# Kernel optimization log

Measured on AMD Instinct MI355X. Metric: run time of the kernel, lower is better.

The kernel has to match this reference:

```python
import jax, jax.numpy as jnp
import numpy as np

N_NODES = 50000
N_EDGES = 1600000
IN_FEAT = 256
HID = IN_FEAT // 2  # 128
OUT_FEAT = 256


def setup_inputs() -> dict:
    key = jax.random.key(0)
    ks = jax.random.split(key, 10)
    x = jax.random.normal(ks[0], (N_NODES, IN_FEAT), dtype=jnp.float32)
    w = jax.random.uniform(ks[1], (N_EDGES, 1), dtype=jnp.float32)
    src = jax.random.randint(ks[2], (N_EDGES,), 0, N_NODES, dtype=jnp.int32)
    dst = jax.random.randint(ks[3], (N_EDGES,), 0, N_NODES, dtype=jnp.int32)
    s = 1.0 / np.sqrt(IN_FEAT)
    W_node = jax.random.uniform(ks[4], (IN_FEAT, HID), jnp.float32, -s, s)
    b_node = jax.random.uniform(ks[5], (HID,), jnp.float32, -s, s)
    W_edge = jax.random.uniform(ks[6], (IN_FEAT, HID), jnp.float32, -s, s)
    b_edge = jax.random.uniform(ks[7], (HID,), jnp.float32, -s, s)
    s2 = 1.0 / np.sqrt(HID)
    W_mlp = jax.random.uniform(ks[8], (HID, OUT_FEAT), jnp.float32, -s2, s2)
    b_mlp = jax.random.uniform(ks[9], (OUT_FEAT,), jnp.float32, -s2, s2)
    return {"x": x, "w": w, "src": src, "dst": dst,
            "W_node": W_node, "b_node": b_node,
            "W_edge": W_edge, "b_edge": b_edge,
            "W_mlp": W_mlp, "b_mlp": b_mlp}


def reference(x, w, src, dst, W_node, b_node, W_edge, b_edge, W_mlp, b_mlp):
    # message[v] = sum_{(u->v) in E} x[u] * w_e   (src_mul_edge + sum)
    message = jax.ops.segment_sum(x[src] * w, dst, num_segments=x.shape[0])  # [N, in_feat]
    h = (x @ W_node + b_node) + (message @ W_edge + b_edge)  # [N, in_feat//2]
    # NOTE: original uses nn.LeakyReLU(True) -> negative_slope=1.0 (identity);
    # replicated faithfully.
    h = jax.nn.leaky_relu(h, negative_slope=1.0)
    return h @ W_mlp + b_mlp  # [N, out_feat]
```

## Files before the change

kernel.cpp:

```cpp
#include <hip/hip_runtime.h>


constexpr int N_NODES  = 50000;
constexpr int N_EDGES  = 1600000;
constexpr int IN_FEAT  = 256;
constexpr int HID      = 128;
constexpr int OUT_FEAT = 256;

constexpr int BIN_SZ   = 32;
constexpr int N_BINS   = (N_NODES + BIN_SZ - 1) / BIN_SZ;
constexpr int CAPBIN   = 1536;
constexpr int EPB      = 4096;
constexpr int N_CBLK   = (N_EDGES + EPB - 1) / EPB;

typedef __attribute__((ext_vector_type(8))) short bf16x8;
typedef __attribute__((ext_vector_type(4))) float f32x4;

static __device__ __forceinline__ unsigned short f2bf(float f) {
    unsigned u = __builtin_bit_cast(unsigned, f);
    u += 0x7FFF + ((u >> 16) & 1);
    return (unsigned short)(u >> 16);
}
static __device__ __forceinline__ float bflo(unsigned u) {
    return __builtin_bit_cast(float, u << 16);
}
static __device__ __forceinline__ float bfhi(unsigned u) {
    return __builtin_bit_cast(float, u & 0xFFFF0000u);
}

__global__ __launch_bounds__(256) void k0_convert(
    const float* __restrict__ Wn, const float* __restrict__ We,
    const float* __restrict__ Wm,
    unsigned short* __restrict__ Wcat_t, unsigned short* __restrict__ Wmt)
{
    int n = blockIdx.x;
    int k = threadIdx.x;
    float v = (n < HID) ? Wn[(size_t)k * HID + n] : We[(size_t)k * HID + (n - HID)];
    Wcat_t[(size_t)n * IN_FEAT + k] = f2bf(v);
    if (k < HID) Wmt[(size_t)n * HID + k] = f2bf(Wm[(size_t)k * OUT_FEAT + n]);
}

__global__ __launch_bounds__(512) void binC(
    const int* __restrict__ src, const int* __restrict__ dst,
    const float* __restrict__ w, int* __restrict__ cursor,
    int2* __restrict__ entries)
{
    __shared__ int  hist[N_BINS];
    __shared__ int  gbase[N_BINS];
    __shared__ int  wsum[8];
    __shared__ int  stot;
    __shared__ int2 sorted[EPB];

    const int t = threadIdx.x;
    const int wave = t >> 6, lane = t & 63;
    const int e0 = blockIdx.x * EPB;

    for (int i = t; i < N_BINS; i += 512) hist[i] = 0;
    __syncthreads();

    int meta[8], wb[8], rk[8], bn[8];
    #pragma unroll
    for (int k = 0; k < 8; ++k) {
        int e = e0 + t + k * 512;
        bn[k] = -1;
        if (e < N_EDGES) {
            int d = dst[e];
            int b = d >> 5;
            bn[k]   = b;
            meta[k] = src[e] | ((d & 31) << 16) | (b << 21);
            wb[k]   = __float_as_int(w[e]);
            rk[k]   = atomicAdd(&hist[b], 1);
        }
    }
    __syncthreads();

    const int b4 = t * 4;
    int c0 = 0, c1 = 0, c2 = 0, c3 = 0;
    if (b4 + 0 < N_BINS) c0 = hist[b4 + 0];
    if (b4 + 1 < N_BINS) c1 = hist[b4 + 1];
    if (b4 + 2 < N_BINS) c2 = hist[b4 + 2];
    if (b4 + 3 < N_BINS) c3 = hist[b4 + 3];
    const int s = c0 + c1 + c2 + c3;
    int pre = s;
    #pragma unroll
    for (int off = 1; off < 64; off <<= 1) {
        int o = __shfl_up(pre, off, 64);
        if (lane >= off) pre += o;
    }
    if (lane == 63) wsum[wave] = pre;
    __syncthreads();
    if (t == 0) {
        int r = 0;
        #pragma unroll
        for (int q = 0; q < 8; ++q) { int v = wsum[q]; wsum[q] = r; r += v; }
        stot = r;
    }
    __syncthreads();
    const int tb = wsum[wave] + pre - s;

    if (b4 + 0 < N_BINS) {
        hist[b4 + 0]  = tb;
        gbase[b4 + 0] = c0 ? atomicAdd(&cursor[b4 + 0], c0) : 0;
    }
    if (b4 + 1 < N_BINS) {
        hist[b4 + 1]  = tb + c0;
        gbase[b4 + 1] = c1 ? atomicAdd(&cursor[b4 + 1], c1) : 0;
    }
    if (b4 + 2 < N_BINS) {
        hist[b4 + 2]  = tb + c0 + c1;
        gbase[b4 + 2] = c2 ? atomicAdd(&cursor[b4 + 2], c2) : 0;
    }
    if (b4 + 3 < N_BINS) {
        hist[b4 + 3]  = tb + c0 + c1 + c2;
        gbase[b4 + 3] = c3 ? atomicAdd(&cursor[b4 + 3], c3) : 0;
    }
    __syncthreads();

    #pragma unroll
    for (int k = 0; k < 8; ++k)
        if (bn[k] >= 0)
            sorted[hist[bn[k]] + rk[k]] = make_int2(meta[k], wb[k]);
    __syncthreads();

    const int tot = stot;
    #pragma unroll
    for (int k = 0; k < 8; ++k) {
        int i = t + k * 512;
        if (i < tot) {
            int2 q = sorted[i];
            int b = ((unsigned)q.x) >> 21;
            int r = i - hist[b];
            int g = gbase[b] + r;
            if (g < CAPBIN)
                entries[(size_t)b * CAPBIN + g] = make_int2(q.x & 0x1FFFFF, q.y);
        }
    }
}

__global__ __launch_bounds__(512) void gatherB(
    const unsigned short* __restrict__ ybf, const float* __restrict__ h0,
    const int* __restrict__ cursor, const int2* __restrict__ entries,
    unsigned short* __restrict__ hbf)
{
    __shared__ int2 sorted[CAPBIN];
    __shared__ int  cnt32[BIN_SZ];
    __shared__ int  offs32[BIN_SZ];

    const int t = threadIdx.x;
    const int bin = blockIdx.x;
    const int node0 = bin * BIN_SZ;
    const int wave = t >> 6, lane = t & 63;

    const int tot = min(cursor[bin], CAPBIN);
    if (t < BIN_SZ) cnt32[t] = 0;
    __syncthreads();

    int2 held[3];
    int  hrank[3], hdloc[3];
    #pragma unroll
    for (int k = 0; k < 3; ++k) {
        hdloc[k] = -1;
        int g = t + k * 512;
        if (g < tot) {
            int2 ep = entries[(size_t)bin * CAPBIN + g];
            int dloc = ep.x >> 16;
            held[k]  = make_int2(ep.x & 0xFFFF, ep.y);
            hdloc[k] = dloc;
            hrank[k] = atomicAdd(&cnt32[dloc], 1);
        }
    }
    __syncthreads();

    if (wave == 0) {
        int v = (lane < BIN_SZ) ? cnt32[lane] : 0;
        int sum = v;
        #pragma unroll
        for (int off = 1; off < BIN_SZ; off <<= 1) {
            int o = __shfl_up(sum, off, 64);
            if (lane >= off) sum += o;
        }
        if (lane < BIN_SZ) offs32[lane] = sum - v;
    }
    __syncthreads();

    #pragma unroll
    for (int k = 0; k < 3; ++k)
        if (hdloc[k] >= 0)
            sorted[offs32[hdloc[k]] + hrank[k]] = held[k];
    __syncthreads();

    #pragma unroll
    for (int n4 = 0; n4 < 4; ++n4) {
        const int nl = wave * 4 + n4;
        const int node = node0 + nl;
        const int beg = offs32[nl];
        const int c = cnt32[nl];
        float a0 = 0.f, a1 = 0.f;
        int j = 0;
        for (; j + 4 <= c; j += 4) {
            int2 q0 = sorted[beg + j];
            int2 q1 = sorted[beg + j + 1];
            int2 q2 = sorted[beg + j + 2];
            int2 q3 = sorted[beg + j + 3];
            unsigned u0 = *(const unsigned*)&ybf[(size_t)q0.x * HID + 2 * lane];
            unsigned u1 = *(const unsigned*)&ybf[(size_t)q1.x * HID + 2 * lane];
            unsigned u2 = *(const unsigned*)&ybf[(size_t)q2.x * HID + 2 * lane];
            unsigned u3 = *(const unsigned*)&ybf[(size_t)q3.x * HID + 2 * lane];
            float w0 = __int_as_float(q0.y), w1 = __int_as_float(q1.y);
            float w2 = __int_as_float(q2.y), w3 = __int_as_float(q3.y);
            a0 += w0 * bflo(u0); a1 += w0 * bfhi(u0);
            a0 += w1 * bflo(u1); a1 += w1 * bfhi(u1);
            a0 += w2 * bflo(u2); a1 += w2 * bfhi(u2);
            a0 += w3 * bflo(u3); a1 += w3 * bfhi(u3);
        }
        for (; j < c; ++j) {
            int2 q = sorted[beg + j];
            unsigned u = *(const unsigned*)&ybf[(size_t)q.x * HID + 2 * lane];
            float wq = __int_as_float(q.y);
            a0 += wq * bflo(u); a1 += wq * bfhi(u);
        }
        if (node < N_NODES) {
            float2 hv = *(const float2*)&h0[(size_t)node * HID + 2 * lane];
            unsigned r = ((unsigned)f2bf(hv.y + a1) << 16)
                       | (unsigned)f2bf(hv.x + a0);
            *(unsigned*)&hbf[(size_t)node * HID + 2 * lane] = r;
        }
    }
}

__global__ __launch_bounds__(256) void gemm1(
    const float* __restrict__ x, const unsigned short* __restrict__ Wcat_t,
    const float* __restrict__ bn, const float* __restrict__ be,
    float* __restrict__ h0, unsigned short* __restrict__ ybf)
{
    __shared__ unsigned short As[128][128];
    __shared__ unsigned short Bs[128][128];
    const int t = threadIdx.x;
    const int m0 = blockIdx.x * 128;
    const int nhalf = blockIdx.y;
    const int n0r = nhalf * 128;

    const int wave = t >> 6, lane = t & 63;
    const int wm = wave & 1, wn = wave >> 1;
    const int la = lane & 15, kq = lane >> 4;

    f32x4 acc[4][4];
    const f32x4 zero = {0.f, 0.f, 0.f, 0.f};
    #pragma unroll
    for (int i = 0; i < 4; ++i)
        #pragma unroll
        for (int j = 0; j < 4; ++j) acc[i][j] = zero;

    const float4* xg = (const float4*)x;
    const float4* bg = (const float4*)Wcat_t;

    for (int kh = 0; kh < 2; ++kh) {
        if (kh) __syncthreads();
        #pragma unroll
        for (int i = 0; i < 16; ++i) {
            int f4  = t + i * 256;
            int row = f4 >> 5;
            int c4  = f4 & 31;
            int node = m0 + row;
            float4 v = make_float4(0.f, 0.f, 0.f, 0.f);
            if (node < N_NODES) v = xg[(size_t)node * 64 + kh * 32 + c4];
            ushort4 b;
            b.x = f2bf(v.x); b.y = f2bf(v.y); b.z = f2bf(v.z); b.w = f2bf(v.w);
            *(ushort4*)&As[row][c4 * 4] = b;
        }
        #pragma unroll
        for (int i = 0; i < 8; ++i) {
            int f4  = t + i * 256;
            int row = f4 >> 4;
            int c4  = f4 & 15;
            ((float4*)&Bs[0][0])[f4] = bg[(size_t)(n0r + row) * 32 + kh * 16 + c4];
        }
        __syncthreads();

        #pragma unroll
        for (int ks = 0; ks < 4; ++ks) {
            int k = ks * 32 + kq * 8;
            bf16x8 a[4], b[4];
            #pragma unroll
            for (int i = 0; i < 4; ++i)
                a[i] = *(const bf16x8*)&As[wm * 64 + i * 16 + la][k];
            #pragma unroll
            for (int j = 0; j < 4; ++j)
                b[j] = *(const bf16x8*)&Bs[wn * 64 + j * 16 + la][k];
            #pragma unroll
            for (int i = 0; i < 4; ++i)
                #pragma unroll
                for (int j = 0; j < 4; ++j)
                    acc[i][j] = __builtin_amdgcn_mfma_f32_16x16x32_bf16(
                        a[i], b[j], acc[i][j], 0, 0, 0);
        }
    }

    float bias[4];
    if (nhalf == 0) {
        #pragma unroll
        for (int j = 0; j < 4; ++j) {
            int n = wn * 64 + j * 16 + la;
            bias[j] = bn[n] + be[n];
        }
    }
    #pragma unroll
    for (int i = 0; i < 4; ++i) {
        int mbase = m0 + wm * 64 + i * 16 + kq * 4;
        #pragma unroll
        for (int j = 0; j < 4; ++j) {
            int n = wn * 64 + j * 16 + la;
            #pragma unroll
            for (int r = 0; r < 4; ++r) {
                int m = mbase + r;
                if (m < N_NODES) {
                    if (nhalf == 0)
                        h0[(size_t)m * HID + n] = acc[i][j][r] + bias[j];
                    else
                        ybf[(size_t)m * HID + n] = f2bf(acc[i][j][r]);
                }
            }
        }
    }
}

__global__ __launch_bounds__(256) void gemm2(
    const unsigned short* __restrict__ hbf, const unsigned short* __restrict__ Wmt,
    const float* __restrict__ bm, float* __restrict__ out)
{
    __shared__ unsigned short As[128][128];
    __shared__ unsigned short Bs[128][128];
    const int t = threadIdx.x;
    const int m0 = blockIdx.x * 128;
    const int n0 = blockIdx.y * 128;

    const float4* ag = (const float4*)hbf;
    #pragma unroll
    for (int i = 0; i < 8; ++i) {
        int f4  = t + i * 256;
        int row = f4 >> 4;
        int node = m0 + row;
        float4 v = make_float4(0.f, 0.f, 0.f, 0.f);
        if (node < N_NODES) v = ag[(size_t)node * 16 + (f4 & 15)];
        ((float4*)&As[0][0])[f4] = v;
    }
    const float4* bg = (const float4*)(Wmt + (size_t)n0 * HID);
    #pragma unroll
    for (int i = 0; i < 8; ++i)
        ((float4*)&Bs[0][0])[t + i * 256] = bg[t + i * 256];
    __syncthreads();

    const int wave = t >> 6, lane = t & 63;
    const int wm = wave & 1, wn = wave >> 1;
    const int la = lane & 15, kq = lane >> 4;

    f32x4 acc[4][4];
    const f32x4 zero = {0.f, 0.f, 0.f, 0.f};
    #pragma unroll
    for (int i = 0; i < 4; ++i)
        #pragma unroll
        for (int j = 0; j < 4; ++j) acc[i][j] = zero;

    #pragma unroll
    for (int ks = 0; ks < 4; ++ks) {
        int k = ks * 32 + kq * 8;
        bf16x8 a[4], b[4];
        #pragma unroll
        for (int i = 0; i < 4; ++i)
            a[i] = *(const bf16x8*)&As[wm * 64 + i * 16 + la][k];
        #pragma unroll
        for (int j = 0; j < 4; ++j)
            b[j] = *(const bf16x8*)&Bs[wn * 64 + j * 16 + la][k];
        #pragma unroll
        for (int i = 0; i < 4; ++i)
            #pragma unroll
            for (int j = 0; j < 4; ++j)
                acc[i][j] = __builtin_amdgcn_mfma_f32_16x16x32_bf16(
                    a[i], b[j], acc[i][j], 0, 0, 0);
    }

    #pragma unroll
    for (int i = 0; i < 4; ++i) {
        int mbase = m0 + wm * 64 + i * 16 + kq * 4;
        #pragma unroll
        for (int j = 0; j < 4; ++j) {
            int n = n0 + wn * 64 + j * 16 + la;
            float b = bm[n];
            #pragma unroll
            for (int r = 0; r < 4; ++r) {
                int m = mbase + r;
                if (m < N_NODES)
                    out[(size_t)m * OUT_FEAT + n] = acc[i][j][r] + b;
            }
        }
    }
}

extern "C" void kernel_launch(void* const* d_in, const int* in_sizes, int n_in,
                              void* d_out, int out_size, void* d_ws, size_t ws_size,
                              hipStream_t stream) {
    const float* x   = (const float*)d_in[0];
    const float* w   = (const float*)d_in[1];
    const int*   src = (const int*)d_in[2];
    const int*   dst = (const int*)d_in[3];
    const float* Wn  = (const float*)d_in[4];
    const float* bn  = (const float*)d_in[5];
    const float* We  = (const float*)d_in[6];
    const float* be  = (const float*)d_in[7];
    const float* Wm  = (const float*)d_in[8];
    const float* bm  = (const float*)d_in[9];
    float* out = (float*)d_out;

    char* p = (char*)d_ws;
    float*          h0      = (float*)p;          p += (size_t)N_NODES * HID * 4;
    unsigned short* ybf     = (unsigned short*)p; p += (size_t)N_NODES * HID * 2;
    unsigned short* hbf     = (unsigned short*)p; p += (size_t)N_NODES * HID * 2;
    int2*           entries = (int2*)p;           p += (size_t)N_BINS * CAPBIN * 8;
    unsigned short* Wcat_t  = (unsigned short*)p; p += (size_t)256 * IN_FEAT * 2;
    unsigned short* Wmt     = (unsigned short*)p; p += (size_t)OUT_FEAT * HID * 2;
    int*            cursor  = (int*)p;            p += (size_t)N_BINS * 4;

    const int grid_m = (N_NODES + 127) / 128;
    dim3 blk(256);

    hipMemsetAsync(cursor, 0, (size_t)N_BINS * 4, stream);
    k0_convert<<<256, blk, 0, stream>>>(Wn, We, Wm, Wcat_t, Wmt);
    binC<<<N_CBLK, dim3(512), 0, stream>>>(src, dst, w, cursor, entries);
    gemm1<<<dim3(grid_m, 2), blk, 0, stream>>>(x, Wcat_t, bn, be, h0, ybf);
    gatherB<<<N_BINS, dim3(512), 0, stream>>>(ybf, h0, cursor, entries, hbf);
    gemm2<<<dim3(grid_m, 2), blk, 0, stream>>>(hbf, Wmt, bm, out);
}
```

Baseline: 281.4 us.

## Halve GEMM LDS tiles with XOR-swizzled layout and raise occupancy

Both GEMM kernels now stage K in 64-wide chunks instead of 128, which halves shared memory per block to 32 KB. They also store tiles with an XOR swizzle on 16-byte columns so the bf16x8 fragment reads avoid LDS bank conflicts. Launch bounds now request 4 blocks per CU. The aim is more resident blocks to hide global latency and cheaper LDS reads, at the cost of more K iterations and barriers per block.

```diff
diff --git a/kernel.cpp b/kernel.cpp
--- a/kernel.cpp
+++ b/kernel.cpp
@@ -14,6 +14,7 @@
 constexpr int N_CBLK   = (N_EDGES + EPB - 1) / EPB;
 
 typedef __attribute__((ext_vector_type(8))) short bf16x8;
+typedef __attribute__((ext_vector_type(8))) unsigned short u16x8;
 typedef __attribute__((ext_vector_type(4))) float f32x4;
 
 static __device__ __forceinline__ unsigned short f2bf(float f) {
@@ -228,13 +229,13 @@
     }
 }
 
-__global__ __launch_bounds__(256) void gemm1(
+__global__ __launch_bounds__(256, 4) void gemm1(
     const float* __restrict__ x, const unsigned short* __restrict__ Wcat_t,
     const float* __restrict__ bn, const float* __restrict__ be,
     float* __restrict__ h0, unsigned short* __restrict__ ybf)
 {
-    __shared__ unsigned short As[128][128];
-    __shared__ unsigned short Bs[128][128];
+    __shared__ unsigned short As[128][64];
+    __shared__ unsigned short Bs[128][64];
     const int t = threadIdx.x;
     const int m0 = blockIdx.x * 128;
     const int nhalf = blockIdx.y;
@@ -252,41 +253,46 @@
         for (int j = 0; j < 4; ++j) acc[i][j] = zero;
 
     const float4* xg = (const float4*)x;
-    const float4* bg = (const float4*)Wcat_t;
-
-    for (int kh = 0; kh < 2; ++kh) {
-        if (kh) __syncthreads();
-        #pragma unroll
-        for (int i = 0; i < 16; ++i) {
-            int f4  = t + i * 256;
-            int row = f4 >> 5;
-            int c4  = f4 & 31;
+    const int srow = t >> 3, sc8 = t & 7;
+
+    for (int kt = 0; kt < 4; ++kt) {
+        if (kt) __syncthreads();
+        #pragma unroll
+        for (int i = 0; i < 4; ++i) {
+            int row = srow + i * 32;
             int node = m0 + row;
-            float4 v = make_float4(0.f, 0.f, 0.f, 0.f);
-            if (node < N_NODES) v = xg[(size_t)node * 64 + kh * 32 + c4];
-            ushort4 b;
-            b.x = f2bf(v.x); b.y = f2bf(v.y); b.z = f2bf(v.z); b.w = f2bf(v.w);
-            *(ushort4*)&As[row][c4 * 4] = b;
-        }
-        #pragma unroll
-        for (int i = 0; i < 8; ++i) {
-            int f4  = t + i * 256;
-            int row = f4 >> 4;
-            int c4  = f4 & 15;
-            ((float4*)&Bs[0][0])[f4] = bg[(size_t)(n0r + row) * 32 + kh * 16 + c4];
+            float4 v0 = make_float4(0.f, 0.f, 0.f, 0.f), v1 = v0;
+            if (node < N_NODES) {
+                v0 = xg[(size_t)node * 64 + kt * 16 + sc8 * 2];
+                v1 = xg[(size_t)node * 64 + kt * 16 + sc8 * 2 + 1];
+            }
+            u16x8 b;
+            b[0] = f2bf(v0.x); b[1] = f2bf(v0.y); b[2] = f2bf(v0.z); b[3] = f2bf(v0.w);
+            b[4] = f2bf(v1.x); b[5] = f2bf(v1.y); b[6] = f2bf(v1.z); b[7] = f2bf(v1.w);
+            *(u16x8*)&As[row][(sc8 ^ (row & 7)) * 8] = b;
+        }
+        #pragma unroll
+        for (int i = 0; i < 4; ++i) {
+            int row = srow + i * 32;
+            float4 v = *(const float4*)(
+                Wcat_t + (size_t)(n0r + row) * IN_FEAT + kt * 64 + sc8 * 8);
+            *(float4*)&Bs[row][(sc8 ^ (row & 7)) * 8] = v;
         }
         __syncthreads();
 
         #pragma unroll
-        for (int ks = 0; ks < 4; ++ks) {
-            int k = ks * 32 + kq * 8;
+        for (int ks = 0; ks < 2; ++ks) {
             bf16x8 a[4], b[4];
             #pragma unroll
-            for (int i = 0; i < 4; ++i)
-                a[i] = *(const bf16x8*)&As[wm * 64 + i * 16 + la][k];
-            #pragma unroll
-            for (int j = 0; j < 4; ++j)
-                b[j] = *(const bf16x8*)&Bs[wn * 64 + j * 16 + la][k];
+            for (int i = 0; i < 4; ++i) {
+                int row = wm * 64 + i * 16 + la;
+                a[i] = *(const bf16x8*)&As[row][((ks * 4 + kq) ^ (row & 7)) * 8];
+            }
+            #pragma unroll
+            for (int j = 0; j < 4; ++j) {
+                int row = wn * 64 + j * 16 + la;
+                b[j] = *(const bf16x8*)&Bs[row][((ks * 4 + kq) ^ (row & 7)) * 8];
+            }
             #pragma unroll
             for (int i = 0; i < 4; ++i)
                 #pragma unroll
@@ -324,35 +330,20 @@
     }
 }
 
-__global__ __launch_bounds__(256) void gemm2(
+__global__ __launch_bounds__(256, 4) void gemm2(
     const unsigned short* __restrict__ hbf, const unsigned short* __restrict__ Wmt,
     const float* __restrict__ bm, float* __restrict__ out)
 {
-    __shared__ unsigned short As[128][128];
-    __shared__ unsigned short Bs[128][128];
+    __shared__ unsigned short As[128][64];
+    __shared__ unsigned short Bs[128][64];
     const int t = threadIdx.x;
     const int m0 = blockIdx.x * 128;
     const int n0 = blockIdx.y * 128;
 
-    const float4* ag = (const float4*)hbf;
-    #pragma unroll
-    for (int i = 0; i < 8; ++i) {
-        int f4  = t + i * 256;
-        int row = f4 >> 4;
-        int node = m0 + row;
-        float4 v = make_float4(0.f, 0.f, 0.f, 0.f);
-        if (node < N_NODES) v = ag[(size_t)node * 16 + (f4 & 15)];
-        ((float4*)&As[0][0])[f4] = v;
-    }
-    const float4* bg = (const float4*)(Wmt + (size_t)n0 * HID);
-    #pragma unroll
-    for (int i = 0; i < 8; ++i)
-        ((float4*)&Bs[0][0])[t + i * 256] = bg[t + i * 256];
-    __syncthreads();
-
     const int wave = t >> 6, lane = t & 63;
     const int wm = wave & 1, wn = wave >> 1;
     const int la = lane & 15, kq = lane >> 4;
+    const int srow = t >> 3, sc8 = t & 7;
 
     f32x4 acc[4][4];
     const f32x4 zero = {0.f, 0.f, 0.f, 0.f};
@@ -361,22 +352,40 @@
         #pragma unroll
         for (int j = 0; j < 4; ++j) acc[i][j] = zero;
 
-    #pragma unroll
-    for (int ks = 0; ks < 4; ++ks) {
-        int k = ks * 32 + kq * 8;
-        bf16x8 a[4], b[4];
-        #pragma unroll
-        for (int i = 0; i < 4; ++i)
-            a[i] = *(const bf16x8*)&As[wm * 64 + i * 16 + la][k];
-        #pragma unroll
-        for (int j = 0; j < 4; ++j)
-            b[j] = *(const bf16x8*)&Bs[wn * 64 + j * 16 + la][k];
-        #pragma unroll
-        for (int i = 0; i < 4; ++i)
-            #pragma unroll
-            for (int j = 0; j < 4; ++j)
-                acc[i][j] = __builtin_amdgcn_mfma_f32_16x16x32_bf16(
-                    a[i], b[j], acc[i][j], 0, 0, 0);
+    for (int kt = 0; kt < 2; ++kt) {
+        if (kt) __syncthreads();
+        #pragma unroll
+        for (int i = 0; i < 4; ++i) {
+            int row = srow + i * 32;
+            int node = m0 + row;
+            if (node >= N_NODES) node = N_NODES - 1;
+            float4 va = *(const float4*)(hbf + (size_t)node * HID + kt * 64 + sc8 * 8);
+            float4 vb = *(const float4*)(Wmt + (size_t)(n0 + row) * HID + kt * 64 + sc8 * 8);
+            *(float4*)&As[row][(sc8 ^ (row & 7)) * 8] = va;
+            *(float4*)&Bs[row][(sc8 ^ (row & 7)) * 8] = vb;
+        }
+        __syncthreads();
+
+        #pragma unroll
+        for (int ks = 0; ks < 2; ++ks) {
+            bf16x8 a[4], b[4];
+            #pragma unroll
+            for (int i = 0; i < 4; ++i) {
+                int row = wm * 64 + i * 16 + la;
+                a[i] = *(const bf16x8*)&As[row][((ks * 4 + kq) ^ (row & 7)) * 8];
+            }
+            #pragma unroll
+            for (int j = 0; j < 4; ++j) {
+                int row = wn * 64 + j * 16 + la;
+                b[j] = *(const bf16x8*)&Bs[row][((ks * 4 + kq) ^ (row & 7)) * 8];
+            }
+            #pragma unroll
+            for (int i = 0; i < 4; ++i)
+                #pragma unroll
+                for (int j = 0; j < 4; ++j)
+                    acc[i][j] = __builtin_amdgcn_mfma_f32_16x16x32_bf16(
+                        a[i], b[j], acc[i][j], 0, 0, 0);
+        }
     }
 
     #pragma unroll
```

Measured after the change: 268.8 us. 1.05x faster.
